# Optimization experiments

Hardware: AMD Instinct MI355X
Metric: run time of the kernel (lower is better)

The kernel has to match this reference:

```python
import jax, jax.numpy as jnp
import numpy as np

WS = 7          # window_size
H = W = 56      # spatial side (L = 3136)
C = 384         # dim
NH = 12         # num_heads
HD = C // NH    # head_dim = 32
HID = 4 * C     # mlp hidden
EPS = 1e-5


def _layernorm(x, g, b):
    m = jnp.mean(x, axis=-1, keepdims=True)
    v = jnp.mean((x - m) ** 2, axis=-1, keepdims=True)
    return (x - m) * jax.lax.rsqrt(v + EPS) * g + b


def _rel_pos_index():
    # Swin relative position index for a WSxWS window -> (WS*WS, WS*WS) int32 in [0, (2WS-1)^2)
    coords = np.stack(np.meshgrid(np.arange(WS), np.arange(WS), indexing='ij')).reshape(2, -1)
    rel = (coords[:, :, None] - coords[:, None, :]).transpose(1, 2, 0)  # (N, N, 2)
    rel = rel + (WS - 1)
    idx = rel[:, :, 0] * (2 * WS - 1) + rel[:, :, 1]
    return jnp.asarray(idx, dtype=jnp.int32)


def setup_inputs() -> dict:
    key = jax.random.key(0)
    ks = jax.random.split(key, 12)
    B = 32
    L = H * W

    def w(k, shape, fan_in):
        return (jax.random.normal(k, shape, jnp.float32) * (fan_in ** -0.5)).astype(jnp.float32)

    return {
        'x': jax.random.normal(ks[0], (B, L, C), jnp.float32),
        'norm1_g': jnp.ones((C,), jnp.float32),
        'norm1_b': jnp.zeros((C,), jnp.float32),
        'qkv_w': w(ks[1], (3 * C, C), C),
        'qkv_b': jnp.zeros((3 * C,), jnp.float32),
        'rel_bias_table': jax.random.normal(ks[2], ((2 * WS - 1) ** 2, NH), jnp.float32) * 0.02,
        'rel_index': _rel_pos_index(),
        'proj_w': w(ks[3], (C, C), C),
        'proj_b': jnp.zeros((C,), jnp.float32),
        'norm2_g': jnp.ones((C,), jnp.float32),
        'norm2_b': jnp.zeros((C,), jnp.float32),
        'fc1_w': w(ks[4], (HID, C), C),
        'fc1_b': jnp.zeros((HID,), jnp.float32),
        'fc2_w': w(ks[5], (C, HID), HID),
        'fc2_b': jnp.zeros((C,), jnp.float32),
    }


def reference(x, norm1_g, norm1_b, qkv_w, qkv_b, rel_bias_table, rel_index,
              proj_w, proj_b, norm2_g, norm2_b, fc1_w, fc1_b, fc2_w, fc2_b):
    B, L, Cc = x.shape
    N = WS * WS
    # window partition: (B,H,W,C) -> (nW*B, N, C)
    xw = x.reshape(B, H // WS, WS, W // WS, WS, Cc)
    xw = xw.transpose(0, 1, 3, 2, 4, 5).reshape(-1, N, Cc)
    # NOTE: original code reassigns x_windows = norm1(x_windows), so residuals
    # branch from the NORMALIZED windows (faithful to source).
    xw = _layernorm(xw, norm1_g, norm1_b)
    # windowed multi-head self-attention with relative position bias
    qkv = (xw @ qkv_w.T + qkv_b).reshape(-1, N, 3, NH, HD).transpose(2, 0, 3, 1, 4)
    q, k, v = qkv[0], qkv[1], qkv[2]              # (nWB, NH, N, HD)
    attn = jnp.einsum('whnd,whmd->whnm', q * (HD ** -0.5), k)
    bias = rel_bias_table[rel_index.reshape(-1)].reshape(N, N, NH).transpose(2, 0, 1)
    attn = jax.nn.softmax(attn + bias[None], axis=-1)
    out = jnp.einsum('whnm,whmd->whnd', attn, v).transpose(0, 2, 1, 3).reshape(-1, N, Cc)
    out = out @ proj_w.T + proj_b
    xw = xw + out
    # MLP block
    h = _layernorm(xw, norm2_g, norm2_b)
    h = jax.nn.gelu(h @ fc1_w.T + fc1_b, approximate=False)
    xw = xw + (h @ fc2_w.T + fc2_b)
    # window reverse -> (B, L, C)
    xw = xw.reshape(B, H // WS, W // WS, WS, WS, Cc)
    return xw.transpose(0, 1, 3, 2, 4, 5).reshape(B, L, Cc)
```

## Files before the change

### kernel.cpp

```cpp
#include <hip/hip_runtime.h>
#include <hip/hip_bf16.h>
#include <math.h>

#define BF16 __hip_bfloat16

typedef __bf16 bf16x8 __attribute__((ext_vector_type(8)));
typedef float  f32x4  __attribute__((ext_vector_type(4)));

__device__ __forceinline__ float bf2f(BF16 v) { return (float)v; }
__device__ __forceinline__ float ldv(const float* p, size_t i) { return p[i]; }
__device__ __forceinline__ float ldv(const BF16* p, size_t i) { return bf2f(p[i]); }
__device__ __forceinline__ void stv(float* p, size_t i, float v) { p[i] = v; }
__device__ __forceinline__ void stv(BF16* p, size_t i, float v) { p[i] = __float2bfloat16(v); }

__device__ __forceinline__ void gload_lds16(const void* g, void* l) {
  __builtin_amdgcn_global_load_lds(
      (const __attribute__((address_space(1))) void*)g,
      (__attribute__((address_space(3))) void*)l, 16, 0, 0);
}

__device__ __forceinline__ float fast_gelu(float v) {
  float u = v * v;
  float z = v * (0.797884561f + 0.0356774081f * u);
  float az = fabsf(z);
  float t = __expf(-2.0f * az);
  float r = (1.0f - t) * __builtin_amdgcn_rcpf(1.0f + t);
  r = copysignf(r, z);
  return 0.5f * v * (1.0f + r);
}

__global__ void write_sentinel(float* out, float val) {
  if (threadIdx.x == 0 && blockIdx.x == 0) out[0] = val;
}

__global__ __launch_bounds__(256) void sanitize(float* __restrict__ out, long long n) {
  long long i0 = (long long)blockIdx.x * 256 + threadIdx.x;
  long long step = (long long)gridDim.x * 256;
  for (long long i = i0; i < n; i += step) {
    unsigned u = __float_as_uint(out[i]);
    if ((u & 0x7F800000u) == 0x7F800000u) out[i] = 131072.0f;
  }
}

__global__ __launch_bounds__(256) void cvt_bf16(const float* __restrict__ src,
                                                __bf16* __restrict__ dst, int n) {
  int i0 = blockIdx.x * 256 + threadIdx.x;
  int step = gridDim.x * 256;
  for (int i = i0; i < n; i += step) dst[i] = (__bf16)src[i];
}

template<bool PART, typename TX>
__global__ __launch_bounds__(256) void ln_kernel(const TX* __restrict__ X,
                                                 const float* __restrict__ G,
                                                 const float* __restrict__ Bt,
                                                 BF16* __restrict__ Y, int row0) {
  const int wave = threadIdx.x >> 6, lane = threadIdx.x & 63;
  const int row = blockIdx.x * 4 + wave;
  size_t src;
  if (PART) {
    int rg = row0 + row;
    int nw = rg / 49, t = rg - nw * 49;
    int b = nw >> 6, wh = (nw >> 3) & 7, ww = nw & 7;
    int i = t / 7, j = t - i * 7;
    int l = (wh * 7 + i) * 56 + ww * 7 + j;
    src = ((size_t)b * 3136 + l) * 384;
  } else {
    src = (size_t)row * 384;
  }
  float xv[6];
  float s = 0.f, s2 = 0.f;
#pragma unroll
  for (int j = 0; j < 6; ++j) {
    float v = ldv(X, src + lane + j * 64);
    xv[j] = v; s += v; s2 += v * v;
  }
#pragma unroll
  for (int off = 32; off > 0; off >>= 1) {
    s += __shfl_xor(s, off);
    s2 += __shfl_xor(s2, off);
  }
  const float m  = s * (1.f / 384.f);
  const float vr = s2 * (1.f / 384.f) - m * m;
  const float rs = rsqrtf(fmaxf(vr, 0.f) + 1e-5f);
  const size_t dst = (size_t)row * 384;
#pragma unroll
  for (int j = 0; j < 6; ++j) {
    int c = lane + j * 64;
    float y = (xv[j] - m) * rs * G[c] + Bt[c];
    Y[dst + c] = __float2bfloat16(y);
  }
}

__global__ __launch_bounds__(256) void bias_expand(const int* __restrict__ RI,
                                                   const float* __restrict__ T,
                                                   float* __restrict__ Bg) {
  int idx = blockIdx.x * 256 + threadIdx.x;
  if (idx < 12 * 2401) {
    int h = idx / 2401, r = idx - h * 2401;
    int t = RI[r];
    if (t < 0) t = 0;
    if (t > 168) t = 168;
    Bg[idx] = T[t * 12 + h];
  }
}

__global__ __launch_bounds__(256) void attn_kernel(BF16* __restrict__ QKV,
                                                   const float* __restrict__ Bg) {
  __shared__ float kvs[4][2][49 * 32];
  const int wave = threadIdx.x >> 6, lane = threadIdx.x & 63;
  const int task = blockIdx.x * 4 + wave;
  const int win = task / 12, h = task - win * 12;
  const size_t base = (size_t)win * 49 * 1152 + (size_t)h * 32;
  float* ks = kvs[wave][0];
  float* vs = kvs[wave][1];
  for (int idx = lane; idx < 49 * 32; idx += 64) {
    int t = idx >> 5, d = idx & 31;
    size_t g = base + (size_t)t * 1152 + d;
    ks[idx] = bf2f(QKV[g + 384]);
    vs[idx] = bf2f(QKV[g + 768]);
  }
  __syncthreads();
  const int n = lane < 49 ? lane : 48;
  float q[32];
  {
    const BF16* qp = QKV + base + (size_t)n * 1152;
#pragma unroll
    for (int d = 0; d < 32; ++d) q[d] = bf2f(qp[d]) * 0.17677669529663687f;
  }
  const float* bp = Bg + h * 2401 + n * 49;
  float mx = -1e30f, lsum = 0.f;
  float O[32];
#pragma unroll
  for (int d = 0; d < 32; ++d) O[d] = 0.f;

  for (int c0 = 0; c0 < 49; c0 += 7) {
    float sv[7];
#pragma unroll
    for (int i = 0; i < 7; ++i) {
      const float* kr = ks + (c0 + i) * 32;
      float a = 0.f;
#pragma unroll
      for (int d = 0; d < 32; ++d) a += q[d] * kr[d];
      sv[i] = a + bp[c0 + i];
    }
    float cm = mx;
#pragma unroll
    for (int i = 0; i < 7; ++i) cm = fmaxf(cm, sv[i]);
    const float sc = __expf(mx - cm);
    float p[7]; float ps = 0.f;
#pragma unroll
    for (int i = 0; i < 7; ++i) { p[i] = __expf(sv[i] - cm); ps += p[i]; }
    lsum = lsum * sc + ps;
    mx = cm;
#pragma unroll
    for (int d = 0; d < 32; ++d) {
      float a = O[d] * sc;
#pragma unroll
      for (int i = 0; i < 7; ++i) a += p[i] * vs[(c0 + i) * 32 + d];
      O[d] = a;
    }
  }
  __syncthreads();
  if (lane < 49) {
    const float inv = 1.f / lsum;
    BF16* op = QKV + ((size_t)win * 49 + n) * 1152 + h * 32;
#pragma unroll
    for (int d = 0; d < 32; ++d) op[d] = __float2bfloat16(O[d] * inv);
  }
}

template<int EPI, typename TC>
__global__ __launch_bounds__(256) void gemm_bt(const BF16* __restrict__ A,
                                               const __bf16* __restrict__ W,
                                               const float* __restrict__ Bias,
                                               const BF16* __restrict__ Res,
                                               TC* __restrict__ C,
                                               int N, int K, int lda, int row0) {
  __shared__ __bf16 sA[2 * 128 * 32];
  __shared__ __bf16 sB[2 * 128 * 32];
  const int tiles_n = N >> 7;
  int bid;
  {
    const int nwg = gridDim.x;
    const int xcd = blockIdx.x & 7, idx = blockIdx.x >> 3;
    const int q = nwg >> 3, r = nwg & 7;
    bid = (xcd < r ? xcd * (q + 1) : r * (q + 1) + (xcd - r) * q) + idx;
  }
  const int tm = bid / tiles_n, tn = bid - tm * tiles_n;
  const int tid = threadIdx.x;
  const int wave = tid >> 6, lane = tid & 63;
  const int lr = lane & 15, q4 = lane >> 4;
  const int wm = (wave >> 1) * 64, wn = (wave & 1) * 64;
  const int srow = tid >> 2, scol = (tid & 3) << 3;

  const BF16*  pa = A + (size_t)(tm * 128 + srow) * lda + scol;
  const __bf16* pb = W + (size_t)(tn * 128 + srow) * K + scol;
  const size_t stepa = (size_t)64 * lda, stepb = (size_t)64 * K;

  __bf16* sAw = sA + wave * 512;
  __bf16* sBw = sB + wave * 512;

  f32x4 acc[4][4];
  const f32x4 fzero = {0.f, 0.f, 0.f, 0.f};
#pragma unroll
  for (int mi = 0; mi < 4; ++mi)
#pragma unroll
    for (int ni = 0; ni < 4; ++ni) acc[mi][ni] = fzero;

  gload_lds16(pa,         sAw);
  gload_lds16(pa + stepa, sAw + 2048);
  gload_lds16(pb,         sBw);
  gload_lds16(pb + stepb, sBw + 2048);
  __syncthreads();

  int cur = 0;
  for (int k0 = 0; k0 < K; k0 += 32) {
    if (k0 + 32 < K) {
      const int nxt = cur ^ 1;
      gload_lds16(pa + (k0 + 32),         sAw + nxt * 4096);
      gload_lds16(pa + (k0 + 32) + stepa, sAw + nxt * 4096 + 2048);
      gload_lds16(pb + (k0 + 32),         sBw + nxt * 4096);
      gload_lds16(pb + (k0 + 32) + stepb, sBw + nxt * 4096 + 2048);
    }
    const __bf16* bufA = sA + cur * 4096;
    const __bf16* bufB = sB + cur * 4096;
    bf16x8 af[4], bfr[4];
#pragma unroll
    for (int i = 0; i < 4; ++i)
      af[i] = *(const bf16x8*)&bufA[(wm + i * 16 + lr) * 32 + q4 * 8];
#pragma unroll
    for (int i = 0; i < 4; ++i)
      bfr[i] = *(const bf16x8*)&bufB[(wn + i * 16 + lr) * 32 + q4 * 8];
#pragma unroll
    for (int mi = 0; mi < 4; ++mi)
#pragma unroll
      for (int ni = 0; ni < 4; ++ni)
        acc[mi][ni] = __builtin_amdgcn_mfma_f32_16x16x32_bf16(af[mi], bfr[ni], acc[mi][ni], 0, 0, 0);
    __syncthreads();
    cur ^= 1;
  }

  float bv[4];
#pragma unroll
  for (int ni = 0; ni < 4; ++ni) bv[ni] = Bias[tn * 128 + wn + ni * 16 + lr];
#pragma unroll
  for (int mi = 0; mi < 4; ++mi) {
#pragma unroll
    for (int r = 0; r < 4; ++r) {
      const int gm = tm * 128 + wm + mi * 16 + q4 * 4 + r;
      size_t out_row;
      if (EPI == 3) {
        int rg = row0 + gm;
        int nw = rg / 49, t = rg - nw * 49;
        int b = nw >> 6, wh = (nw >> 3) & 7, ww = nw & 7;
        int i2 = t / 7, j2 = t - i2 * 7;
        int l = (wh * 7 + i2) * 56 + ww * 7 + j2;
        out_row = (size_t)b * 3136 + l;
      } else {
        out_row = (size_t)gm;
      }
#pragma unroll
      for (int ni = 0; ni < 4; ++ni) {
        const int gn = tn * 128 + wn + ni * 16 + lr;
        float v = acc[mi][ni][r] + bv[ni];
        if (EPI == 1) v = fast_gelu(v);
        if (EPI == 2 || EPI == 3) v += bf2f(Res[(size_t)gm * N + gn]);
        stv(C, out_row * (size_t)N + gn, v);
      }
    }
  }
}

extern "C" void kernel_launch(void* const* d_in, const int* in_sizes, int n_in,
                              void* d_out, int out_size, void* d_ws, size_t ws_size,
                              hipStream_t stream) {
  const float* x      = (const float*)d_in[0];
  const float* n1g    = (const float*)d_in[1];
  const float* n1b    = (const float*)d_in[2];
  const float* qkv_w  = (const float*)d_in[3];
  const float* qkv_b  = (const float*)d_in[4];
  const float* rbt    = (const float*)d_in[5];
  const int*   ridx   = (const int*)d_in[6];
  const float* proj_w = (const float*)d_in[7];
  const float* proj_b = (const float*)d_in[8];
  const float* n2g    = (const float*)d_in[9];
  const float* n2b    = (const float*)d_in[10];
  const float* fc1_w  = (const float*)d_in[11];
  const float* fc1_b  = (const float*)d_in[12];
  const float* fc2_w  = (const float*)d_in[13];
  const float* fc2_b  = (const float*)d_in[14];
  float* out = (float*)d_out;

  double wsMB = (double)ws_size / 1048576.0;
  if (wsMB > 4092.0) wsMB = 4092.0;
  float wsenc = 1.0f + (float)((long long)(wsMB / 4.0)) / 1024.0f;

  bool sizes_ok = (n_in == 15) && (out_size == 38535168);
  const long long M = 100352;
  int nc = 0;
  const int cands[5] = {1, 2, 4, 8, 16};
  for (int i = 0; i < 5; ++i) {
    long long R = M / cands[i];
    if (4608LL * R + 3654400 <= (long long)ws_size) { nc = cands[i]; break; }
  }
  if (!sizes_ok) { write_sentinel<<<1, 64, 0, stream>>>(out, ldexpf(wsenc, 21)); return; }
  if (nc == 0)   { write_sentinel<<<1, 64, 0, stream>>>(out, ldexpf(wsenc, 20)); return; }

  const int R = (int)(M / nc);
  const int T = R >> 7;

  char* ws = (char*)d_ws;
  BF16*   xw_c  = (BF16*)(ws);
  BF16*   qkv_c = (BF16*)(ws + 768LL * R);
  BF16*   xw2_c = (BF16*)(ws + 3840LL * R);
  __bf16* wq    = (__bf16*)(ws + 4608LL * R);
  __bf16* wp    = wq + 442368;
  __bf16* w1    = wp + 147456;
  __bf16* w2    = w1 + 589824;
  float*  bg    = (float*)(ws + 4608LL * R + 3538944);

  cvt_bf16<<<432, 256, 0, stream>>>(qkv_w, wq, 442368);
  cvt_bf16<<<144, 256, 0, stream>>>(proj_w, wp, 147456);
  cvt_bf16<<<576, 256, 0, stream>>>(fc1_w, w1, 589824);
  cvt_bf16<<<576, 256, 0, stream>>>(fc2_w, w2, 589824);
  bias_expand<<<113, 256, 0, stream>>>(ridx, rbt, bg);

  for (int c = 0; c < nc; ++c) {
    const int row0 = c * R;
    ln_kernel<true, float><<<R / 4, 256, 0, stream>>>(x, n1g, n1b, xw_c, row0);
    gemm_bt<0, BF16><<<T * 9, 256, 0, stream>>>(xw_c, wq, qkv_b, nullptr, qkv_c,
                                                1152, 384, 384, 0);
    attn_kernel<<<(R / 49) * 3, 256, 0, stream>>>(qkv_c, bg);
    gemm_bt<2, BF16><<<T * 3, 256, 0, stream>>>(qkv_c, wp, proj_b, xw_c, xw2_c,
                                                384, 384, 1152, 0);
    ln_kernel<false, BF16><<<R / 4, 256, 0, stream>>>(xw2_c, n2g, n2b, xw_c, 0);
    gemm_bt<1, BF16><<<T * 12, 256, 0, stream>>>(xw_c, w1, fc1_b, nullptr, qkv_c,
                                                 1536, 384, 384, 0);
    gemm_bt<3, float><<<T * 3, 256, 0, stream>>>(qkv_c, w2, fc2_b, xw2_c, out,
                                                 384, 1536, 1536, row0);
  }
  sanitize<<<2048, 256, 0, stream>>>(out, 38535168LL);
}
```

Before: 1.223 ms.

## Triple-buffer GEMM LDS pipeline and fold output sanitize into fc2 epilogue

The bf16 GEMM moves from a double-buffered loop with two barriers per k-step to a three-stage buffer. Loads are issued two steps ahead, with an explicit vmcnt wait and a single barrier per iteration. The separate sanitize kernel, which rescanned the whole fp32 output to replace non-finite values, is removed and its check is done in the final GEMM's epilogue before the store. This saves a full read/write pass over the output and reduces sync stalls, at the cost of 50% more LDS per block, which may lower occupancy.

```diff
diff --git a/kernel.cpp b/kernel.cpp
--- a/kernel.cpp
+++ b/kernel.cpp
@@ -31,15 +31,6 @@
 
 __global__ void write_sentinel(float* out, float val) {
   if (threadIdx.x == 0 && blockIdx.x == 0) out[0] = val;
-}
-
-__global__ __launch_bounds__(256) void sanitize(float* __restrict__ out, long long n) {
-  long long i0 = (long long)blockIdx.x * 256 + threadIdx.x;
-  long long step = (long long)gridDim.x * 256;
-  for (long long i = i0; i < n; i += step) {
-    unsigned u = __float_as_uint(out[i]);
-    if ((u & 0x7F800000u) == 0x7F800000u) out[i] = 131072.0f;
-  }
 }
 
 __global__ __launch_bounds__(256) void cvt_bf16(const float* __restrict__ src,
@@ -176,8 +167,8 @@
                                                const BF16* __restrict__ Res,
                                                TC* __restrict__ C,
                                                int N, int K, int lda, int row0) {
-  __shared__ __bf16 sA[2 * 128 * 32];
-  __shared__ __bf16 sB[2 * 128 * 32];
+  __shared__ __bf16 sA[3 * 4096];
+  __shared__ __bf16 sB[3 * 4096];
   const int tiles_n = N >> 7;
   int bid;
   {
@@ -200,6 +191,19 @@
   __bf16* sAw = sA + wave * 512;
   __bf16* sBw = sB + wave * 512;
 
+  const int nsteps = K >> 5;
+
+  auto STAGE = [&](int t, int b) {
+    const BF16*   qa = pa + t * 32;
+    const __bf16* qb = pb + t * 32;
+    __bf16* da = sAw + b * 4096;
+    __bf16* db = sBw + b * 4096;
+    gload_lds16(qa,         da);
+    gload_lds16(qa + stepa, da + 2048);
+    gload_lds16(qb,         db);
+    gload_lds16(qb + stepb, db + 2048);
+  };
+
   f32x4 acc[4][4];
   const f32x4 fzero = {0.f, 0.f, 0.f, 0.f};
 #pragma unroll
@@ -207,23 +211,21 @@
 #pragma unroll
     for (int ni = 0; ni < 4; ++ni) acc[mi][ni] = fzero;
 
-  gload_lds16(pa,         sAw);
-  gload_lds16(pa + stepa, sAw + 2048);
-  gload_lds16(pb,         sBw);
-  gload_lds16(pb + stepb, sBw + 2048);
-  __syncthreads();
-
-  int cur = 0;
-  for (int k0 = 0; k0 < K; k0 += 32) {
-    if (k0 + 32 < K) {
-      const int nxt = cur ^ 1;
-      gload_lds16(pa + (k0 + 32),         sAw + nxt * 4096);
-      gload_lds16(pa + (k0 + 32) + stepa, sAw + nxt * 4096 + 2048);
-      gload_lds16(pb + (k0 + 32),         sBw + nxt * 4096);
-      gload_lds16(pb + (k0 + 32) + stepb, sBw + nxt * 4096 + 2048);
+  STAGE(0, 0);
+  STAGE(1, 1);
+
+  int bc = 0;
+  int bn = 2;
+  for (int t = 0; t < nsteps; ++t) {
+    if (t + 1 < nsteps) {
+      asm volatile("s_waitcnt vmcnt(4)" ::: "memory");
+    } else {
+      asm volatile("s_waitcnt vmcnt(0)" ::: "memory");
     }
-    const __bf16* bufA = sA + cur * 4096;
-    const __bf16* bufB = sB + cur * 4096;
+    __builtin_amdgcn_s_barrier();
+    if (t + 2 < nsteps) STAGE(t + 2, bn);
+    const __bf16* bufA = sA + bc * 4096;
+    const __bf16* bufB = sB + bc * 4096;
     bf16x8 af[4], bfr[4];
 #pragma unroll
     for (int i = 0; i < 4; ++i)
@@ -236,8 +238,8 @@
 #pragma unroll
       for (int ni = 0; ni < 4; ++ni)
         acc[mi][ni] = __builtin_amdgcn_mfma_f32_16x16x32_bf16(af[mi], bfr[ni], acc[mi][ni], 0, 0, 0);
-    __syncthreads();
-    cur ^= 1;
+    if (++bc == 3) bc = 0;
+    if (++bn == 3) bn = 0;
   }
 
   float bv[4];
@@ -265,6 +267,10 @@
         float v = acc[mi][ni][r] + bv[ni];
         if (EPI == 1) v = fast_gelu(v);
         if (EPI == 2 || EPI == 3) v += bf2f(Res[(size_t)gm * N + gn]);
+        if (EPI == 3) {
+          unsigned u = __float_as_uint(v);
+          if ((u & 0x7F800000u) == 0x7F800000u) v = 131072.0f;
+        }
         stv(C, out_row * (size_t)N + gn, v);
       }
     }
@@ -339,5 +345,4 @@
     gemm_bt<3, float><<<T * 3, 256, 0, stream>>>(qkv_c, w2, fc2_b, xw2_c, out,
                                                  384, 1536, 1536, row0);
   }
-  sanitize<<<2048, 256, 0, stream>>>(out, 38535168LL);
-}
+}
```

After: 1.186 ms. 3.1% less time.
